# Performance work log

Measured on AMD Instinct MI355X. Metric: run time of the kernel, lower is better.

Reference implementation:

```python
import jax, jax.numpy as jnp
import numpy as np

B, L, D, H = 4, 1024, 1024, 16
HD = D // H
SCALE = 1.0 / np.sqrt(HD)
NOISE_PROB = 0.05
NOISE_SCALE = 0.1


def _linear(x, w, b):
    # torch nn.Linear convention: y = x @ W^T + b, W: [out, in]
    return x @ w.T + b


def _quantum_noise(key, real, imag, p=NOISE_PROB, s=NOISE_SCALE):
    """Phase flips, amplitude noise, and measurement dropout on a complex
    tensor represented as (real, imag). Deterministic given `key`."""
    k_phase, k_amp, k_nr, k_ni, k_meas = jax.random.split(key, 5)
    shape = real.shape
    flip = jnp.where(jax.random.uniform(k_phase, shape) < p, -1.0, 1.0)
    amp_mask = (jax.random.uniform(k_amp, shape) < p).astype(real.dtype)
    new_r = real * flip + jax.random.normal(k_nr, shape, real.dtype) * s * amp_mask
    new_i = imag * flip + jax.random.normal(k_ni, shape, imag.dtype) * s * amp_mask
    keep = 1.0 - (jax.random.uniform(k_meas, shape) < p * 0.5).astype(real.dtype)
    return new_r * keep, new_i * keep


def _heads(t):
    # [B, L, D] -> [B, H, L, HD]
    b, l, _ = t.shape
    return t.reshape(b, l, H, HD).transpose(0, 2, 1, 3)


def setup_inputs() -> dict:
    key = jax.random.key(0)
    ks = jax.random.split(key, 16)
    inp = {
        "x_real": jax.random.normal(ks[0], (B, L, D), jnp.float32),
        "x_imag": jax.random.normal(ks[1], (B, L, D), jnp.float32),
        "mask": jnp.ones((B, L), jnp.int32),
    }
    names = ["qr", "qi", "kr", "ki", "vr", "vi", "or", "oi"]
    for i, n in enumerate(names):
        inp[n + "_w"] = jax.random.normal(ks[2 + i], (D, D), jnp.float32) * 0.02
        inp[n + "_b"] = jnp.zeros((D,), jnp.float32)
    ent = jnp.eye(H) + (jax.random.normal(ks[10], (H, H)) * 0.1) * (
        jax.random.uniform(ks[11], (H, H)) < 0.2
    ).astype(jnp.float32)
    inp["ent"] = ent
    return inp


def reference(x_real, x_imag, mask, qr_w, qr_b, qi_w, qi_b, kr_w, kr_b,
              ki_w, ki_b, vr_w, vr_b, vi_w, vi_b, or_w, or_b, oi_w, oi_b, ent):
    # complex Q/K/V: real part from x.real, imag part from x.imag
    q_r, q_i = _linear(x_real, qr_w, qr_b), _linear(x_imag, qi_w, qi_b)
    k_r, k_i = _linear(x_real, kr_w, kr_b), _linear(x_imag, ki_w, ki_b)
    v_r, v_i = _linear(x_real, vr_w, vr_b), _linear(x_imag, vi_w, vi_b)

    nkey = jax.random.key(1)
    q_r, q_i = _quantum_noise(jax.random.fold_in(nkey, 0), q_r, q_i)
    k_r, k_i = _quantum_noise(jax.random.fold_in(nkey, 1), k_r, k_i)
    v_r, v_i = _quantum_noise(jax.random.fold_in(nkey, 2), v_r, v_i)

    q_r, q_i, k_r, k_i, v_r, v_i = map(_heads, (q_r, q_i, k_r, k_i, v_r, v_i))

    # torch.einsum('bhld,hh->bhld') == per-head scaling by diag(ent)
    d = jnp.diagonal(ent)[None, :, None, None]
    q_r, q_i = q_r * d, q_i * d
    k_r, k_i = k_r * d, k_i * d

    # Re(q . conj(k)) interference score: [B, H, Lq, Lk]
    scores = (jnp.einsum("bhqd,bhkd->bhqk", q_r, k_r)
              + jnp.einsum("bhqd,bhkd->bhqk", q_i, k_i)) * SCALE
    scores = jnp.where(mask[:, None, None, :] == 0, -1e9, scores)
    attn = jax.nn.softmax(scores, axis=-1)

    out_r = jnp.einsum("bhqk,bhkd->bhqd", attn, v_r)
    out_i = jnp.einsum("bhqk,bhkd->bhqd", attn, v_i)
    out_r = out_r.transpose(0, 2, 1, 3).reshape(x_real.shape)
    out_i = out_i.transpose(0, 2, 1, 3).reshape(x_real.shape)

    out_real = _linear(out_r, or_w, or_b)
    out_imag = _linear(out_i, oi_w, oi_b)
    return out_real, out_imag, attn
```

## Files before the change

### kernel.cpp

```cpp
#include <hip/hip_runtime.h>
#include <cstdint>

#define PARTITIONABLE 1

static constexpr int Bsz = 4, Lsz = 1024, Dsz = 1024, Hn = 16, HDsz = 64;
static constexpr size_t ELEMS = (size_t)Bsz * Lsz * Dsz;
static constexpr uint32_t HALF_N = (uint32_t)(ELEMS / 2);
static constexpr float SCALE = 0.125f;
static constexpr float P_NOISE = 0.05f;
static constexpr float S_NOISE = 0.1f;
static constexpr size_t MBy = 1024 * 1024;

typedef unsigned short u16;
typedef uint64_t u64;
typedef __attribute__((ext_vector_type(8))) short short8v;
typedef __attribute__((ext_vector_type(4))) float floatx4;
typedef __attribute__((ext_vector_type(4))) unsigned int uint4v;

__device__ __forceinline__ void gload16(const u16* g, u16* l) {
  __builtin_amdgcn_global_load_lds(
      (const __attribute__((address_space(1))) void*)(g),
      (__attribute__((address_space(3))) void*)(l), 16, 0, 0);
}

__host__ __device__ __forceinline__ void tf2x32(uint32_t k0, uint32_t k1,
                                                uint32_t x0, uint32_t x1,
                                                uint32_t& o0, uint32_t& o1) {
  uint32_t ks2 = k0 ^ k1 ^ 0x1BD11BDAu;
  x0 += k0; x1 += k1;
#define TFR(r) { x0 += x1; x1 = (x1 << (r)) | (x1 >> (32 - (r))); x1 ^= x0; }
  TFR(13) TFR(15) TFR(26) TFR(6)
  x0 += k1; x1 += ks2 + 1u;
  TFR(17) TFR(29) TFR(16) TFR(24)
  x0 += ks2; x1 += k0 + 2u;
  TFR(13) TFR(15) TFR(26) TFR(6)
  x0 += k0; x1 += k1 + 3u;
  TFR(17) TFR(29) TFR(16) TFR(24)
  x0 += k1; x1 += ks2 + 4u;
  TFR(13) TFR(15) TFR(26) TFR(6)
  x0 += ks2; x1 += k0 + 5u;
#undef TFR
  o0 = x0; o1 = x1;
}

struct KeySet { uint32_t k[5][2]; };
struct AllKeys { KeySet t[3]; };

__device__ __forceinline__ uint32_t draw_bits(uint32_t k0, uint32_t k1, uint32_t idx) {
#if PARTITIONABLE
  uint32_t o0, o1; tf2x32(k0, k1, 0u, idx, o0, o1);
  return o0 ^ o1;
#else
  uint32_t o0, o1;
  if (idx < HALF_N) { tf2x32(k0, k1, idx, idx + HALF_N, o0, o1); return o0; }
  tf2x32(k0, k1, idx - HALF_N, idx, o0, o1); return o1;
#endif
}

__device__ __forceinline__ float unif01(uint32_t bits) {
  return __uint_as_float((bits >> 9) | 0x3f800000u) - 1.0f;
}

__device__ __forceinline__ float normal_from_bits(uint32_t bits) {
  const float LO = -0.99999994f;
  float f = unif01(bits);
  float x = fmaxf(LO, f * 2.0f + LO);
  float w = -log1pf(-x * x);
  float p;
  if (w < 5.0f) {
    w = w - 2.5f;
    p = 2.81022636e-08f;
    p = fmaf(p, w, 3.43273939e-07f);
    p = fmaf(p, w, -3.5233877e-06f);
    p = fmaf(p, w, -4.39150654e-06f);
    p = fmaf(p, w, 0.00021858087f);
    p = fmaf(p, w, -0.00125372503f);
    p = fmaf(p, w, -0.00417768164f);
    p = fmaf(p, w, 0.246640727f);
    p = fmaf(p, w, 1.50140941f);
  } else {
    w = sqrtf(w) - 3.0f;
    p = -0.000200214257f;
    p = fmaf(p, w, 0.000100950558f);
    p = fmaf(p, w, 0.00134934322f);
    p = fmaf(p, w, -0.00367342844f);
    p = fmaf(p, w, 0.00573950773f);
    p = fmaf(p, w, -0.0076224613f);
    p = fmaf(p, w, 0.00943887047f);
    p = fmaf(p, w, 1.00167406f);
    p = fmaf(p, w, 2.83297682f);
  }
  return 1.41421356f * (p * x);
}

__device__ __forceinline__ uint32_t bf16_rn(float f) {
  uint32_t u = __float_as_uint(f);
  return (u + 0x7FFFu + ((u >> 16) & 1u)) >> 16;
}
__device__ __forceinline__ float bf2f(uint32_t h) { return __uint_as_float(h << 16); }
__device__ __forceinline__ void cvt_split(float4 v, u64& hi, u64& lo) {
  uint32_t h0 = bf16_rn(v.x), h1 = bf16_rn(v.y), h2 = bf16_rn(v.z), h3 = bf16_rn(v.w);
  float r0 = v.x - bf2f(h0), r1 = v.y - bf2f(h1), r2 = v.z - bf2f(h2), r3 = v.w - bf2f(h3);
  uint32_t l0 = bf16_rn(r0), l1 = bf16_rn(r1), l2 = bf16_rn(r2), l3 = bf16_rn(r3);
  hi = (u64)h0 | ((u64)h1 << 16) | ((u64)h2 << 32) | ((u64)h3 << 48);
  lo = (u64)l0 | ((u64)l1 << 16) | ((u64)l2 << 32) | ((u64)l3 << 48);
}

__device__ __forceinline__ void mfma_tile(const u16* Ahs, const u16* Als,
                                          const u16* Bhs, const u16* Bls,
                                          int l, int wm, int wn, floatx4 acc[4][4]) {
#pragma unroll
  for (int c = 0; c < 2; ++c) {
    const int pr = (l ^ (l >> 4) ^ (c << 2)) & 63;
    short8v aH[4], aL[4], bH[4], bL[4];
#pragma unroll
    for (int t = 0; t < 4; ++t) {
      const int ia = ((c * 8 + wm * 4 + t) * 64 + pr) * 8;
      aH[t] = *(const short8v*)&Ahs[ia]; aL[t] = *(const short8v*)&Als[ia];
      const int ib = ((c * 8 + wn * 4 + t) * 64 + pr) * 8;
      bH[t] = *(const short8v*)&Bhs[ib]; bL[t] = *(const short8v*)&Bls[ib];
    }
#pragma unroll
    for (int mt = 0; mt < 4; ++mt)
#pragma unroll
      for (int nt = 0; nt < 4; ++nt) {
        acc[mt][nt] = __builtin_amdgcn_mfma_f32_16x16x32_bf16(aH[mt], bH[nt], acc[mt][nt], 0, 0, 0);
        acc[mt][nt] = __builtin_amdgcn_mfma_f32_16x16x32_bf16(aH[mt], bL[nt], acc[mt][nt], 0, 0, 0);
        acc[mt][nt] = __builtin_amdgcn_mfma_f32_16x16x32_bf16(aL[mt], bH[nt], acc[mt][nt], 0, 0, 0);
      }
  }
}

__device__ __forceinline__ void mfma_step(const u16* Ahs, const u16* Als,
                                          const u16* Bhs, const u16* Bls,
                                          int pr, int wm, int wn, floatx4 acc[4][4]) {
  short8v aH[4], aL[4], bH[4], bL[4];
#pragma unroll
  for (int t = 0; t < 4; ++t) {
    const int ia = ((wm * 4 + t) * 64 + pr) * 8;
    aH[t] = *(const short8v*)&Ahs[ia]; aL[t] = *(const short8v*)&Als[ia];
    const int ib = ((wn * 4 + t) * 64 + pr) * 8;
    bH[t] = *(const short8v*)&Bhs[ib]; bL[t] = *(const short8v*)&Bls[ib];
  }
#pragma unroll
  for (int mt = 0; mt < 4; ++mt)
#pragma unroll
    for (int nt = 0; nt < 4; ++nt) {
      acc[mt][nt] = __builtin_amdgcn_mfma_f32_16x16x32_bf16(aH[mt], bH[nt], acc[mt][nt], 0, 0, 0);
      acc[mt][nt] = __builtin_amdgcn_mfma_f32_16x16x32_bf16(aH[mt], bL[nt], acc[mt][nt], 0, 0, 0);
      acc[mt][nt] = __builtin_amdgcn_mfma_f32_16x16x32_bf16(aL[mt], bH[nt], acc[mt][nt], 0, 0, 0);
    }
}

struct SJob { const float* src; u16* dh; u16* dl; int n4; };
struct SJobs { SJob j[8]; };

__global__ __launch_bounds__(256) void split8_kernel(SJobs js) {
  const SJob J = js.j[blockIdx.y];
  int i = blockIdx.x * 256 + (int)threadIdx.x;
  if (i >= J.n4) return;
  float4 v = ((const float4*)J.src)[i];
  u64 h, l; cvt_split(v, h, l);
  ((u64*)J.dh)[i] = h; ((u64*)J.dl)[i] = l;
}

struct GJob3 { const u16* Ah; const u16* Al;
               const u16* Wh[3]; const u16* Wl[3];
               const float* bias[3]; u16* Yh[3]; u16* Yl[3]; };
struct GJobs3 { GJob3 j[2]; };

__global__ __launch_bounds__(256, 2) void gemm3_kernel(GJobs3 jobs) {
  const GJob3 J = jobs.j[blockIdx.z];
  const int n0 = blockIdx.x * 128, m0 = blockIdx.y * 128;
  __shared__ u16 Ahs[4096], Als[4096];
  __shared__ u16 Bhs[3][4096], Bls[3][4096];
  const int tid = (int)threadIdx.x, w = tid >> 6, l = tid & 63;
  const int wm = w >> 1, wn = w & 1;
  const int qA = (l ^ (l >> 4)) & 15, colA = (l >> 4) * 8;
  const int pr = (l ^ (l >> 4)) & 63;
  const int t0 = w * 2, t1 = w * 2 + 1;

  const u16* ahp = J.Ah + (size_t)(m0 + qA) * Dsz + colA;
  const u16* alp = J.Al + (size_t)(m0 + qA) * Dsz + colA;
  const u16* whp0 = J.Wh[0] + (size_t)(n0 + qA) * Dsz + colA;
  const u16* wlp0 = J.Wl[0] + (size_t)(n0 + qA) * Dsz + colA;
  const u16* whp1 = J.Wh[1] + (size_t)(n0 + qA) * Dsz + colA;
  const u16* wlp1 = J.Wl[1] + (size_t)(n0 + qA) * Dsz + colA;
  const u16* whp2 = J.Wh[2] + (size_t)(n0 + qA) * Dsz + colA;
  const u16* wlp2 = J.Wl[2] + (size_t)(n0 + qA) * Dsz + colA;

  floatx4 acc[3][4][4];
#pragma unroll
  for (int z = 0; z < 3; ++z)
#pragma unroll
    for (int i = 0; i < 4; ++i)
#pragma unroll
      for (int j = 0; j < 4; ++j) acc[z][i][j] = (floatx4){0.f, 0.f, 0.f, 0.f};

  for (int kt = 0; kt < 32; ++kt) {
    const size_t g0 = (size_t)(t0 * 16) * Dsz + (size_t)kt * 32;
    const size_t g1 = (size_t)(t1 * 16) * Dsz + (size_t)kt * 32;
    __syncthreads();
    gload16(ahp + g0, &Ahs[t0 * 512]);  gload16(ahp + g1, &Ahs[t1 * 512]);
    gload16(alp + g0, &Als[t0 * 512]);  gload16(alp + g1, &Als[t1 * 512]);
    gload16(whp0 + g0, &Bhs[0][t0 * 512]); gload16(whp0 + g1, &Bhs[0][t1 * 512]);
    gload16(wlp0 + g0, &Bls[0][t0 * 512]); gload16(wlp0 + g1, &Bls[0][t1 * 512]);
    gload16(whp1 + g0, &Bhs[1][t0 * 512]); gload16(whp1 + g1, &Bhs[1][t1 * 512]);
    gload16(wlp1 + g0, &Bls[1][t0 * 512]); gload16(wlp1 + g1, &Bls[1][t1 * 512]);
    gload16(whp2 + g0, &Bhs[2][t0 * 512]); gload16(whp2 + g1, &Bhs[2][t1 * 512]);
    gload16(wlp2 + g0, &Bls[2][t0 * 512]); gload16(wlp2 + g1, &Bls[2][t1 * 512]);
    __syncthreads();

    short8v aH[4], aL[4];
#pragma unroll
    for (int t = 0; t < 4; ++t) {
      const int ia = ((wm * 4 + t) * 64 + pr) * 8;
      aH[t] = *(const short8v*)&Ahs[ia]; aL[t] = *(const short8v*)&Als[ia];
    }
#pragma unroll
    for (int z = 0; z < 3; ++z) {
#pragma unroll
      for (int nt = 0; nt < 4; ++nt) {
        const int ib = ((wn * 4 + nt) * 64 + pr) * 8;
        short8v bH = *(const short8v*)&Bhs[z][ib];
        short8v bL = *(const short8v*)&Bls[z][ib];
#pragma unroll
        for (int mt = 0; mt < 4; ++mt) {
          acc[z][mt][nt] = __builtin_amdgcn_mfma_f32_16x16x32_bf16(aH[mt], bH, acc[z][mt][nt], 0, 0, 0);
          acc[z][mt][nt] = __builtin_amdgcn_mfma_f32_16x16x32_bf16(aH[mt], bL, acc[z][mt][nt], 0, 0, 0);
          acc[z][mt][nt] = __builtin_amdgcn_mfma_f32_16x16x32_bf16(aL[mt], bH, acc[z][mt][nt], 0, 0, 0);
        }
      }
    }
  }

  const int colLane = l & 15, rquad = l >> 4;
#pragma unroll
  for (int z = 0; z < 3; ++z) {
    u16* Yh = J.Yh[z]; u16* Yl = J.Yl[z];
#pragma unroll
    for (int nt = 0; nt < 4; ++nt) {
      const int col = n0 + wn * 64 + nt * 16 + colLane;
      const float bv = J.bias[z][col];
#pragma unroll
      for (int mt = 0; mt < 4; ++mt) {
        const int r0 = m0 + wm * 64 + mt * 16 + rquad * 4;
#pragma unroll
        for (int j2 = 0; j2 < 4; ++j2) {
          float v = acc[z][mt][nt][j2] + bv;
          const uint32_t hi = bf16_rn(v);
          const uint32_t lo = bf16_rn(v - bf2f(hi));
          Yh[(size_t)(r0 + j2) * Dsz + col] = (u16)hi;
          Yl[(size_t)(r0 + j2) * Dsz + col] = (u16)lo;
        }
      }
    }
  }
}

struct GJob { const u16* Ah; const u16* Al; const u16* Wh; const u16* Wl;
              const float* bias; float* Yf; };
struct GJobs { GJob j[2]; };

__global__ __launch_bounds__(256, 2) void gemm_f32_kernel(GJobs jobs) {
  const GJob J = jobs.j[blockIdx.z];
  const int n0 = blockIdx.x * 128, m0 = blockIdx.y * 128;
  __shared__ u16 Ahs[8192], Als[8192], Bhs[8192], Bls[8192];
  const int tid = (int)threadIdx.x, w = tid >> 6, l = tid & 63;
  const int wm = w >> 1, wn = w & 1;
  const int cA = w >> 1, m2A = l >> 4;
  const int qA = (l ^ m2A ^ (cA << 2)) & 15;
  const int colA = cA * 32 + m2A * 8;
  const int tb = (w & 1) * 4;

  const u16* ahp = J.Ah + (size_t)(m0 + qA) * Dsz + colA;
  const u16* alp = J.Al + (size_t)(m0 + qA) * Dsz + colA;
  const u16* whp = J.Wh + (size_t)(n0 + qA) * Dsz + colA;
  const u16* wlp = J.Wl + (size_t)(n0 + qA) * Dsz + colA;

  floatx4 acc[4][4];
#pragma unroll
  for (int i = 0; i < 4; ++i)
#pragma unroll
    for (int j = 0; j < 4; ++j) acc[i][j] = (floatx4){0.f, 0.f, 0.f, 0.f};

  for (int k0 = 0; k0 < Dsz; k0 += 64) {
    __syncthreads();
#pragma unroll
    for (int i = 0; i < 4; ++i) {
      const size_t go = (size_t)((tb + i) * 16) * Dsz + k0;
      gload16(ahp + go, &Ahs[(w * 4 + i) * 512]);
      gload16(alp + go, &Als[(w * 4 + i) * 512]);
      gload16(whp + go, &Bhs[(w * 4 + i) * 512]);
      gload16(wlp + go, &Bls[(w * 4 + i) * 512]);
    }
    __syncthreads();
    mfma_tile(Ahs, Als, Bhs, Bls, l, wm, wn, acc);
  }

  const int colLane = l & 15, rquad = l >> 4;
#pragma unroll
  for (int nt = 0; nt < 4; ++nt) {
    const int col = n0 + wn * 64 + nt * 16 + colLane;
    const float bv = J.bias[col];
#pragma unroll
    for (int mt = 0; mt < 4; ++mt) {
      const int r0 = m0 + wm * 64 + mt * 16 + rquad * 4;
#pragma unroll
      for (int j2 = 0; j2 < 4; ++j2)
        J.Yf[(size_t)(r0 + j2) * Dsz + col] = acc[mt][nt][j2] + bv;
    }
  }
}

__global__ __launch_bounds__(256) void noise_kernel(
    u16* __restrict__ qhr, u16* __restrict__ qlr, u16* __restrict__ qhi, u16* __restrict__ qli,
    u16* __restrict__ khr, u16* __restrict__ klr, u16* __restrict__ khi, u16* __restrict__ kli,
    u16* __restrict__ vhr, u16* __restrict__ vlr, u16* __restrict__ vhi, u16* __restrict__ vli,
    const float* __restrict__ ent, AllKeys keys) {
  const uint32_t e = blockIdx.x * 256u + threadIdx.x;
  const int j = (int)blockIdx.y;
  u16 *rh, *rl, *ih, *il;
  if (j == 0) { rh = qhr; rl = qlr; ih = qhi; il = qli; }
  else if (j == 1) { rh = khr; rl = klr; ih = khi; il = kli; }
  else { rh = vhr; rl = vlr; ih = vhi; il = vli; }
  const KeySet& ks = keys.t[j];
  const uint32_t b_phase = draw_bits(ks.k[0][0], ks.k[0][1], e);
  const uint32_t b_amp   = draw_bits(ks.k[1][0], ks.k[1][1], e);
  const uint32_t b_nr    = draw_bits(ks.k[2][0], ks.k[2][1], e);
  const uint32_t b_ni    = draw_bits(ks.k[3][0], ks.k[3][1], e);
  const uint32_t b_meas  = draw_bits(ks.k[4][0], ks.k[4][1], e);
  const float flip = (unif01(b_phase) < P_NOISE) ? -1.0f : 1.0f;
  const float amp  = (unif01(b_amp)  < P_NOISE) ? 1.0f : 0.0f;
  const float keep = (unif01(b_meas) < P_NOISE * 0.5f) ? 0.0f : 1.0f;
  const float nr = normal_from_bits(b_nr);
  const float ni = normal_from_bits(b_ni);
  float r  = bf2f(rh[e]) + bf2f(rl[e]);
  float iv = bf2f(ih[e]) + bf2f(il[e]);
  r  = (r  * flip + nr * S_NOISE * amp) * keep;
  iv = (iv * flip + ni * S_NOISE * amp) * keep;
  if (j != 2) {
    const int h = ((int)e & (Dsz - 1)) >> 6;
    const float d = ent[h * Hn + h];
    r *= d; iv *= d;
  }
  uint32_t hr = bf16_rn(r);  rh[e] = (u16)hr; rl[e] = (u16)bf16_rn(r - bf2f(hr));
  uint32_t hi2 = bf16_rn(iv); ih[e] = (u16)hi2; il[e] = (u16)bf16_rn(iv - bf2f(hi2));
}

__global__ __launch_bounds__(256, 2) void scores_kernel(
    const u16* __restrict__ qhr, const u16* __restrict__ qlr,
    const u16* __restrict__ qhi, const u16* __restrict__ qli,
    const u16* __restrict__ khr, const u16* __restrict__ klr,
    const u16* __restrict__ khi, const u16* __restrict__ kli,
    const int* __restrict__ mask, float* __restrict__ attn) {
  const int bh = (int)blockIdx.z;
  const int b = bh >> 4, h = bh & 15;
  const int n0 = blockIdx.x * 128, m0 = blockIdx.y * 128;
  __shared__ u16 Ahs[2][4096], Als[2][4096], Bhs[2][4096], Bls[2][4096];
  const int tid = (int)threadIdx.x, w = tid >> 6, l = tid & 63;
  const int wm = w >> 1, wn = w & 1;
  const int qA = (l ^ (l >> 4)) & 15, colA = (l >> 4) * 8;
  const int pr = (l ^ (l >> 4)) & 63;
  const int t0 = w * 2, t1 = w * 2 + 1;

  const size_t aoff = ((size_t)(b * Lsz) + m0 + qA) * Dsz + h * HDsz + colA;
  const size_t boff = ((size_t)(b * Lsz) + n0 + qA) * Dsz + h * HDsz + colA;

  floatx4 acc[4][4];
#pragma unroll
  for (int i = 0; i < 4; ++i)
#pragma unroll
    for (int j = 0; j < 4; ++j) acc[i][j] = (floatx4){0.f, 0.f, 0.f, 0.f};

#define STGS(bufi, AH, AL, BH, BL, K0V) { \
    const size_t g0 = (size_t)(t0 * 16) * Dsz + (K0V); \
    const size_t g1 = (size_t)(t1 * 16) * Dsz + (K0V); \
    gload16(AH + aoff + g0, &Ahs[bufi][t0 * 512]); gload16(AH + aoff + g1, &Ahs[bufi][t1 * 512]); \
    gload16(AL + aoff + g0, &Als[bufi][t0 * 512]); gload16(AL + aoff + g1, &Als[bufi][t1 * 512]); \
    gload16(BH + boff + g0, &Bhs[bufi][t0 * 512]); gload16(BH + boff + g1, &Bhs[bufi][t1 * 512]); \
    gload16(BL + boff + g0, &Bls[bufi][t0 * 512]); gload16(BL + boff + g1, &Bls[bufi][t1 * 512]); }

  STGS(0, qhr, qlr, khr, klr, 0)
  __syncthreads();
  STGS(1, qhr, qlr, khr, klr, 32)
  mfma_step(Ahs[0], Als[0], Bhs[0], Bls[0], pr, wm, wn, acc);
  __syncthreads();
  STGS(0, qhi, qli, khi, kli, 0)
  mfma_step(Ahs[1], Als[1], Bhs[1], Bls[1], pr, wm, wn, acc);
  __syncthreads();
  STGS(1, qhi, qli, khi, kli, 32)
  mfma_step(Ahs[0], Als[0], Bhs[0], Bls[0], pr, wm, wn, acc);
  __syncthreads();
  mfma_step(Ahs[1], Als[1], Bhs[1], Bls[1], pr, wm, wn, acc);
#undef STGS

  const int colLane = l & 15, rquad = l >> 4;
#pragma unroll
  for (int nt = 0; nt < 4; ++nt) {
    const int col = n0 + wn * 64 + nt * 16 + colLane;
    const int mv = mask[b * Lsz + col];
#pragma unroll
    for (int mt = 0; mt < 4; ++mt) {
      const int r0 = m0 + wm * 64 + mt * 16 + rquad * 4;
#pragma unroll
      for (int j = 0; j < 4; ++j)
        attn[((size_t)bh * Lsz + r0 + j) * Lsz + col] =
            (mv == 0) ? -1e9f : acc[mt][nt][j] * SCALE;
    }
  }
}

__global__ __launch_bounds__(256) void vtrans_kernel(
    const u16* __restrict__ vhr, const u16* __restrict__ vlr,
    const u16* __restrict__ vhi, const u16* __restrict__ vli,
    u16* __restrict__ vth, u16* __restrict__ vtl) {
  const int bh = (int)blockIdx.y;
  const int b = bh >> 4, h = bh & 15;
  const int k0 = blockIdx.x * 64;
  __shared__ uint32_t T[128 * 65];
  const int t = (int)threadIdx.x;
  const int krow = t >> 4, d4 = (t & 15) * 4;

#pragma unroll
  for (int src = 0; src < 2; ++src) {
    const u16* VH = src ? vhi : vhr;
    const u16* VL = src ? vli : vlr;
    const int nb = src * 64;
#pragma unroll
    for (int p = 0; p < 4; ++p) {
      const int k = p * 16 + krow;
      const size_t off = ((size_t)(b * Lsz) + k0 + k) * Dsz + h * HDsz + d4;
      u64 hv = *(const u64*)(VH + off);
      u64 lv = *(const u64*)(VL + off);
#pragma unroll
      for (int e = 0; e < 4; ++e) {
        uint32_t hi = (uint32_t)((hv >> (16 * e)) & 0xFFFFu);
        uint32_t lo = (uint32_t)((lv >> (16 * e)) & 0xFFFFu);
        T[(nb + d4 + e) * 65 + k] = lo | (hi << 16);
      }
    }
  }
  __syncthreads();
  const int n = t >> 1, hf = t & 1;
  const size_t rowb = ((size_t)bh * 128 + n) * Lsz + k0 + hf * 32;
#pragma unroll
  for (int g = 0; g < 4; ++g) {
    uint32_t wv[8];
#pragma unroll
    for (int u = 0; u < 8; ++u) wv[u] = T[n * 65 + hf * 32 + g * 8 + u];
    uint4v hvv, lvv;
    hvv.x = (wv[0] >> 16) | (wv[1] & 0xFFFF0000u);
    hvv.y = (wv[2] >> 16) | (wv[3] & 0xFFFF0000u);
    hvv.z = (wv[4] >> 16) | (wv[5] & 0xFFFF0000u);
    hvv.w = (wv[6] >> 16) | (wv[7] & 0xFFFF0000u);
    lvv.x = (wv[0] & 0xFFFFu) | (wv[1] << 16);
    lvv.y = (wv[2] & 0xFFFFu) | (wv[3] << 16);
    lvv.z = (wv[4] & 0xFFFFu) | (wv[5] << 16);
    lvv.w = (wv[6] & 0xFFFFu) | (wv[7] << 16);
    *(uint4v*)&vth[rowb + g * 8] = hvv;
    *(uint4v*)&vtl[rowb + g * 8] = lvv;
  }
}

__global__ __launch_bounds__(256) void rowstat_kernel(const float* __restrict__ S,
                                                      float* __restrict__ rowm,
                                                      float* __restrict__ rowsum) {
  const int wv = (int)threadIdx.x >> 6, lane = (int)threadIdx.x & 63;
  const size_t row = (size_t)blockIdx.x * 4 + wv;
  const float* p = S + row * Lsz;
  float4 v[4];
#pragma unroll
  for (int i = 0; i < 4; ++i) v[i] = *(const float4*)(p + i * 256 + lane * 4);
  float m = -3.402823466e38f;
#pragma unroll
  for (int i = 0; i < 4; ++i)
    m = fmaxf(m, fmaxf(fmaxf(v[i].x, v[i].y), fmaxf(v[i].z, v[i].w)));
#pragma unroll
  for (int d = 1; d < 64; d <<= 1) m = fmaxf(m, __shfl_xor(m, d));
  float s = 0.f;
#pragma unroll
  for (int i = 0; i < 4; ++i)
    s += expf(v[i].x - m) + expf(v[i].y - m) + expf(v[i].z - m) + expf(v[i].w - m);
#pragma unroll
  for (int d = 1; d < 64; d <<= 1) s += __shfl_xor(s, d);
  if (lane == 0) { rowm[row] = m; rowsum[row] = s; }
}

__global__ __launch_bounds__(256, 2) void pv_kernel(
    float* __restrict__ attn, const u16* __restrict__ vth, const u16* __restrict__ vtl,
    const float* __restrict__ rowm, const float* __restrict__ rowsum,
    u16* __restrict__ ohr, u16* __restrict__ olr,
    u16* __restrict__ ohi, u16* __restrict__ oli) {
  const int bh = (int)blockIdx.y;
  const int b = bh >> 4, h = bh & 15;
  const int m0 = blockIdx.x * 128;
  __shared__ u16 Ahs[2][4096], Als[2][4096], Bhs[2][4096], Bls[2][4096];
  const int tid = (int)threadIdx.x, w = tid >> 6, l = tid & 63;
  const int wm = w >> 1, wn = w & 1;
  const int qA = (l ^ (l >> 4)) & 15, colA = (l >> 4) * 8;
  const int pr = (l ^ (l >> 4)) & 63;
  const int t0 = w * 2, t1 = w * 2 + 1;

  const int ar = tid >> 3, akq = tid & 7;
  const int am2 = akq >> 1, ahalf = akq & 1;
  int aidx[4];
  float rmv[4], inv[4];
#pragma unroll
  for (int rr = 0; rr < 4; ++rr) {
    const int trow = ar + rr * 32;
    const int p = ((trow & 15) + 16 * am2) ^ am2;
    aidx[rr] = ((trow >> 4) * 64 + p) * 8 + ahalf * 4;
    const size_t grow = (size_t)bh * Lsz + m0 + trow;
    rmv[rr] = rowm[grow]; inv[rr] = 1.0f / rowsum[grow];
  }
  float* arp = attn + ((size_t)bh * Lsz + m0 + ar) * Lsz + akq * 4;
  const u16* bhp = vth + ((size_t)bh * 128 + qA) * Lsz + colA;
  const u16* blp = vtl + ((size_t)bh * 128 + qA) * Lsz + colA;

  floatx4 acc[4][4];
#pragma unroll
  for (int i = 0; i < 4; ++i)
#pragma unroll
    for (int j = 0; j < 4; ++j) acc[i][j] = (floatx4){0.f, 0.f, 0.f, 0.f};

#define STGB(bufi, K0V) { \
    const size_t g0 = (size_t)(t0 * 16) * Lsz + (K0V); \
    const size_t g1 = (size_t)(t1 * 16) * Lsz + (K0V); \
    gload16(bhp + g0, &Bhs[bufi][t0 * 512]); gload16(bhp + g1, &Bhs[bufi][t1 * 512]); \
    gload16(blp + g0, &Bls[bufi][t0 * 512]); gload16(blp + g1, &Bls[bufi][t1 * 512]); }

#define LOADA(K0V, A4) { \
    _Pragma("unroll") for (int rr = 0; rr < 4; ++rr) \
      A4[rr] = *(const float4*)(arp + (size_t)(rr * 32) * Lsz + (K0V)); }

#define PROCA(bufi, K0V, A4) { \
    _Pragma("unroll") for (int rr = 0; rr < 4; ++rr) { \
      float4 p4; \
      p4.x = expf(A4[rr].x - rmv[rr]) * inv[rr]; \
      p4.y = expf(A4[rr].y - rmv[rr]) * inv[rr]; \
      p4.z = expf(A4[rr].z - rmv[rr]) * inv[rr]; \
      p4.w = expf(A4[rr].w - rmv[rr]) * inv[rr]; \
      *(float4*)(arp + (size_t)(rr * 32) * Lsz + (K0V)) = p4; \
      u64 h64, l64; cvt_split(p4, h64, l64); \
      *(u64*)&Ahs[bufi][aidx[rr]] = h64; *(u64*)&Als[bufi][aidx[rr]] = l64; } }

  {
    float4 a4[4];
    LOADA(0, a4)
    STGB(0, 0)
    PROCA(0, 0, a4)
  }
  __syncthreads();
  for (int kt = 0; kt < 32; kt += 2) {
    float4 n4[4];
    if (kt + 1 < 32) { LOADA((size_t)(kt + 1) * 32, n4) STGB(1, (size_t)(kt + 1) * 32) }
    mfma_step(Ahs[0], Als[0], Bhs[0], Bls[0], pr, wm, wn, acc);
    if (kt + 1 < 32) PROCA(1, (size_t)(kt + 1) * 32, n4)
    __syncthreads();
    if (kt + 2 < 32) { LOADA((size_t)(kt + 2) * 32, n4) STGB(0, (size_t)(kt + 2) * 32) }
    mfma_step(Ahs[1], Als[1], Bhs[1], Bls[1], pr, wm, wn, acc);
    if (kt + 2 < 32) PROCA(0, (size_t)(kt + 2) * 32, n4)
    __syncthreads();
  }
#undef STGB
#undef LOADA
#undef PROCA

  const int colLane = l & 15, rquad = l >> 4;
#pragma unroll
  for (int nt = 0; nt < 4; ++nt) {
    const int col = wn * 64 + nt * 16 + colLane;
    u16* oh = (col < 64) ? ohr : ohi;
    u16* ol = (col < 64) ? olr : oli;
    const int dcol = col & 63;
#pragma unroll
    for (int mt = 0; mt < 4; ++mt) {
      const int r0 = m0 + wm * 64 + mt * 16 + rquad * 4;
#pragma unroll
      for (int j = 0; j < 4; ++j) {
        float v = acc[mt][nt][j];
        const uint32_t hi = bf16_rn(v);
        const uint32_t lo = bf16_rn(v - bf2f(hi));
        const size_t oidx = ((size_t)(b * Lsz) + r0 + j) * Dsz + h * HDsz + dcol;
        oh[oidx] = (u16)hi; ol[oidx] = (u16)lo;
      }
    }
  }
}

extern "C" void kernel_launch(void* const* d_in, const int* in_sizes, int n_in,
                              void* d_out, int out_size, void* d_ws, size_t ws_size,
                              hipStream_t stream) {
  const float* x_real = (const float*)d_in[0];
  const float* x_imag = (const float*)d_in[1];
  const int*   mask   = (const int*)d_in[2];
  const float* pw[6] = {(const float*)d_in[3], (const float*)d_in[5], (const float*)d_in[7],
                        (const float*)d_in[9], (const float*)d_in[11], (const float*)d_in[13]};
  const float* pb[6] = {(const float*)d_in[4], (const float*)d_in[6], (const float*)d_in[8],
                        (const float*)d_in[10], (const float*)d_in[12], (const float*)d_in[14]};
  const float* or_w = (const float*)d_in[15]; const float* or_b = (const float*)d_in[16];
  const float* oi_w = (const float*)d_in[17]; const float* oi_b = (const float*)d_in[18];
  const float* ent  = (const float*)d_in[19];

  float* out_real = (float*)d_out;
  float* out_imag = out_real + ELEMS;
  float* attn     = out_imag + ELEMS;

  if (ws_size < 96 * MBy) return;
  uint8_t* wsb = (uint8_t*)d_ws;
  u16* qhr = (u16*)(wsb + 0 * MBy);  u16* qlr = (u16*)(wsb + 8 * MBy);
  u16* qhi = (u16*)(wsb + 16 * MBy); u16* qli = (u16*)(wsb + 24 * MBy);
  u16* khr = (u16*)(wsb + 32 * MBy); u16* klr = (u16*)(wsb + 40 * MBy);
  u16* khi = (u16*)(wsb + 48 * MBy); u16* kli = (u16*)(wsb + 56 * MBy);
  u16* xhr = (u16*)(wsb + 64 * MBy); u16* xlr = (u16*)(wsb + 72 * MBy);
  u16* xhi = (u16*)(wsb + 80 * MBy); u16* xli = (u16*)(wsb + 88 * MBy);
  u16* vth = (u16*)(wsb + 64 * MBy); u16* vtl = (u16*)(wsb + 80 * MBy);
  u16* ohr = (u16*)(wsb + 0 * MBy);  u16* olr = (u16*)(wsb + 8 * MBy);
  u16* ohi = (u16*)(wsb + 16 * MBy); u16* oli = (u16*)(wsb + 24 * MBy);
  u16* owh[2] = {(u16*)(wsb + 32 * MBy), (u16*)(wsb + 36 * MBy)};
  u16* owl[2] = {(u16*)(wsb + 34 * MBy), (u16*)(wsb + 38 * MBy)};

  uint8_t* atb = (uint8_t*)attn;
  u16* vhr = (u16*)(atb + 0 * MBy);  u16* vlr = (u16*)(atb + 8 * MBy);
  u16* vhi = (u16*)(atb + 16 * MBy); u16* vli = (u16*)(atb + 24 * MBy);

  float* rowm = out_real;
  float* rowsum = out_real + 65536;

  AllKeys keys;
  for (int j = 0; j < 3; ++j) {
    uint32_t a, b2;
    tf2x32(0u, 1u, 0u, (uint32_t)j, a, b2);
#if PARTITIONABLE
    for (int i = 0; i < 5; ++i)
      tf2x32(a, b2, 0u, (uint32_t)i, keys.t[j].k[i][0], keys.t[j].k[i][1]);
#else
    uint32_t out10[10];
    for (int i = 0; i < 5; ++i) {
      uint32_t o0, o1; tf2x32(a, b2, (uint32_t)i, (uint32_t)(i + 5), o0, o1);
      out10[i] = o0; out10[i + 5] = o1;
    }
    for (int i = 0; i < 5; ++i) { keys.t[j].k[i][0] = out10[2*i]; keys.t[j].k[i][1] = out10[2*i+1]; }
#endif
  }

  u16* pwh[6]; u16* pwl[6];
  for (int z = 0; z < 6; ++z) {
    pwh[z] = (u16*)(atb + 32 * MBy + (size_t)z * 4 * MBy);
    pwl[z] = pwh[z] + (size_t)Dsz * Dsz;
  }
  SJobs sj{};
  sj.j[0] = {x_real, xhr, xlr, (int)(ELEMS / 4)};
  sj.j[1] = {x_imag, xhi, xli, (int)(ELEMS / 4)};
  for (int z = 0; z < 6; ++z) sj.j[2 + z] = {pw[z], pwh[z], pwl[z], Dsz * Dsz / 4};
  split8_kernel<<<dim3(4096, 8), 256, 0, stream>>>(sj);

  GJobs3 pj{};
  pj.j[0].Ah = xhr; pj.j[0].Al = xlr;
  pj.j[0].Wh[0] = pwh[0]; pj.j[0].Wl[0] = pwl[0]; pj.j[0].bias[0] = pb[0];
  pj.j[0].Yh[0] = qhr; pj.j[0].Yl[0] = qlr;
  pj.j[0].Wh[1] = pwh[2]; pj.j[0].Wl[1] = pwl[2]; pj.j[0].bias[1] = pb[2];
  pj.j[0].Yh[1] = khr; pj.j[0].Yl[1] = klr;
  pj.j[0].Wh[2] = pwh[4]; pj.j[0].Wl[2] = pwl[4]; pj.j[0].bias[2] = pb[4];
  pj.j[0].Yh[2] = vhr; pj.j[0].Yl[2] = vlr;
  pj.j[1].Ah = xhi; pj.j[1].Al = xli;
  pj.j[1].Wh[0] = pwh[1]; pj.j[1].Wl[0] = pwl[1]; pj.j[1].bias[0] = pb[1];
  pj.j[1].Yh[0] = qhi; pj.j[1].Yl[0] = qli;
  pj.j[1].Wh[1] = pwh[3]; pj.j[1].Wl[1] = pwl[3]; pj.j[1].bias[1] = pb[3];
  pj.j[1].Yh[1] = khi; pj.j[1].Yl[1] = kli;
  pj.j[1].Wh[2] = pwh[5]; pj.j[1].Wl[2] = pwl[5]; pj.j[1].bias[2] = pb[5];
  pj.j[1].Yh[2] = vhi; pj.j[1].Yl[2] = vli;
  gemm3_kernel<<<dim3(8, 32, 2), 256, 0, stream>>>(pj);

  noise_kernel<<<dim3((uint32_t)(ELEMS / 256), 3), 256, 0, stream>>>(
      qhr, qlr, qhi, qli, khr, klr, khi, kli, vhr, vlr, vhi, vli, ent, keys);

  vtrans_kernel<<<dim3(16, 64), 256, 0, stream>>>(vhr, vlr, vhi, vli, vth, vtl);

  scores_kernel<<<dim3(8, 8, 64), 256, 0, stream>>>(
      qhr, qlr, qhi, qli, khr, klr, khi, kli, mask, attn);

  SJobs so{};
  so.j[0] = {or_w, owh[0], owl[0], Dsz * Dsz / 4};
  so.j[1] = {oi_w, owh[1], owl[1], Dsz * Dsz / 4};
  split8_kernel<<<dim3(1024, 2), 256, 0, stream>>>(so);

  rowstat_kernel<<<dim3(16384), 256, 0, stream>>>(attn, rowm, rowsum);

  pv_kernel<<<dim3(8, 64), 256, 0, stream>>>(attn, vth, vtl, rowm, rowsum,
                                             ohr, olr, ohi, oli);

  GJobs oj{};
  oj.j[0].Ah = ohr; oj.j[0].Al = olr; oj.j[0].Wh = owh[0]; oj.j[0].Wl = owl[0];
  oj.j[0].bias = or_b; oj.j[0].Yf = out_real;
  oj.j[1].Ah = ohi; oj.j[1].Al = oli; oj.j[1].Wh = owh[1]; oj.j[1].Wl = owl[1];
  oj.j[1].bias = oi_b; oj.j[1].Yf = out_imag;
  gemm_f32_kernel<<<dim3(8, 32, 2), 256, 0, stream>>>(oj);
}
```

Baseline: 771.6 us.

## Split noise kernel into two passes, computing Gaussian draws only for amp-flagged elements

The noise pass is split in two. The first kernel applies flip, keep and entanglement scaling, and compacts the indices of elements whose amplitude-noise flag is set (and that are not dropped) into a list using wave ballot plus an atomic counter. The second kernel computes the two normal draws only for those roughly 5% of elements and adds the noise. This removes two Threefry draws and the Box-Muller/erfinv-style normal computations for about 95% of elements. In exchange it adds an extra launch, atomics, and a reread and rewrite of the flagged elements, which incurs a second bf16 rounding on them. The final element order is also nondeterministic.

After: 2.797 ms. 3.63x slower.

```diff
diff --git a/kernel.cpp b/kernel.cpp
--- a/kernel.cpp
+++ b/kernel.cpp
@@ -155,7 +155,8 @@
 struct SJob { const float* src; u16* dh; u16* dl; int n4; };
 struct SJobs { SJob j[8]; };
 
-__global__ __launch_bounds__(256) void split8_kernel(SJobs js) {
+__global__ __launch_bounds__(256) void split8_kernel(SJobs js, uint32_t* counter) {
+  if (counter && blockIdx.x == 0 && blockIdx.y == 0 && threadIdx.x == 0) *counter = 0;
   const SJob J = js.j[blockIdx.y];
   int i = blockIdx.x * 256 + (int)threadIdx.x;
   if (i >= J.n4) return;
@@ -313,11 +314,12 @@
   }
 }
 
-__global__ __launch_bounds__(256) void noise_kernel(
+__global__ __launch_bounds__(256) void noise1_kernel(
     u16* __restrict__ qhr, u16* __restrict__ qlr, u16* __restrict__ qhi, u16* __restrict__ qli,
     u16* __restrict__ khr, u16* __restrict__ klr, u16* __restrict__ khi, u16* __restrict__ kli,
     u16* __restrict__ vhr, u16* __restrict__ vlr, u16* __restrict__ vhi, u16* __restrict__ vli,
-    const float* __restrict__ ent, AllKeys keys) {
+    const float* __restrict__ ent, AllKeys keys,
+    uint32_t* __restrict__ list, uint32_t* __restrict__ counter) {
   const uint32_t e = blockIdx.x * 256u + threadIdx.x;
   const int j = (int)blockIdx.y;
   u16 *rh, *rl, *ih, *il;
@@ -327,25 +329,62 @@
   const KeySet& ks = keys.t[j];
   const uint32_t b_phase = draw_bits(ks.k[0][0], ks.k[0][1], e);
   const uint32_t b_amp   = draw_bits(ks.k[1][0], ks.k[1][1], e);
-  const uint32_t b_nr    = draw_bits(ks.k[2][0], ks.k[2][1], e);
-  const uint32_t b_ni    = draw_bits(ks.k[3][0], ks.k[3][1], e);
   const uint32_t b_meas  = draw_bits(ks.k[4][0], ks.k[4][1], e);
   const float flip = (unif01(b_phase) < P_NOISE) ? -1.0f : 1.0f;
-  const float amp  = (unif01(b_amp)  < P_NOISE) ? 1.0f : 0.0f;
+  const bool  ampf = (unif01(b_amp)  < P_NOISE);
   const float keep = (unif01(b_meas) < P_NOISE * 0.5f) ? 0.0f : 1.0f;
-  const float nr = normal_from_bits(b_nr);
-  const float ni = normal_from_bits(b_ni);
-  float r  = bf2f(rh[e]) + bf2f(rl[e]);
-  float iv = bf2f(ih[e]) + bf2f(il[e]);
-  r  = (r  * flip + nr * S_NOISE * amp) * keep;
-  iv = (iv * flip + ni * S_NOISE * amp) * keep;
+  float d = 1.0f;
   if (j != 2) {
     const int h = ((int)e & (Dsz - 1)) >> 6;
-    const float d = ent[h * Hn + h];
-    r *= d; iv *= d;
-  }
+    d = ent[h * Hn + h];
+  }
+  float r  = (bf2f(rh[e]) + bf2f(rl[e])) * flip * keep * d;
+  float iv = (bf2f(ih[e]) + bf2f(il[e])) * flip * keep * d;
   uint32_t hr = bf16_rn(r);  rh[e] = (u16)hr; rl[e] = (u16)bf16_rn(r - bf2f(hr));
   uint32_t hi2 = bf16_rn(iv); ih[e] = (u16)hi2; il[e] = (u16)bf16_rn(iv - bf2f(hi2));
+
+  const bool flag = ampf && (keep != 0.0f);
+  const int lane = (int)threadIdx.x & 63;
+  unsigned long long mask = __ballot(flag);
+  int cnt = __popcll(mask);
+  int base = 0;
+  if (lane == 0 && cnt) base = (int)atomicAdd(counter, (uint32_t)cnt);
+  base = __shfl(base, 0);
+  if (flag) {
+    int pos = __popcll(mask & ((1ull << lane) - 1ull));
+    list[base + pos] = ((uint32_t)j << 22) | e;
+  }
+}
+
+__global__ __launch_bounds__(256) void noise2_kernel(
+    const uint32_t* __restrict__ list, const uint32_t* __restrict__ counter,
+    u16* __restrict__ qhr, u16* __restrict__ qlr, u16* __restrict__ qhi, u16* __restrict__ qli,
+    u16* __restrict__ khr, u16* __restrict__ klr, u16* __restrict__ khi, u16* __restrict__ kli,
+    u16* __restrict__ vhr, u16* __restrict__ vlr, u16* __restrict__ vhi, u16* __restrict__ vli,
+    const float* __restrict__ ent, AllKeys keys) {
+  const uint32_t cnt = *counter;
+  const uint32_t stride = gridDim.x * 256u;
+  for (uint32_t i = blockIdx.x * 256u + threadIdx.x; i < cnt; i += stride) {
+    const uint32_t pk = list[i];
+    const int j = (int)(pk >> 22);
+    const uint32_t e = pk & 0x3FFFFFu;
+    u16 *rh, *rl, *ih, *il;
+    if (j == 0) { rh = qhr; rl = qlr; ih = qhi; il = qli; }
+    else if (j == 1) { rh = khr; rl = klr; ih = khi; il = kli; }
+    else { rh = vhr; rl = vlr; ih = vhi; il = vli; }
+    const KeySet& ks = keys.t[j];
+    const float nr = normal_from_bits(draw_bits(ks.k[2][0], ks.k[2][1], e));
+    const float ni = normal_from_bits(draw_bits(ks.k[3][0], ks.k[3][1], e));
+    float d = 1.0f;
+    if (j != 2) {
+      const int h = ((int)e & (Dsz - 1)) >> 6;
+      d = ent[h * Hn + h];
+    }
+    float r  = bf2f(rh[e]) + bf2f(rl[e]) + nr * S_NOISE * d;
+    float iv = bf2f(ih[e]) + bf2f(il[e]) + ni * S_NOISE * d;
+    uint32_t hr = bf16_rn(r);  rh[e] = (u16)hr; rl[e] = (u16)bf16_rn(r - bf2f(hr));
+    uint32_t hi2 = bf16_rn(iv); ih[e] = (u16)hi2; il[e] = (u16)bf16_rn(iv - bf2f(hi2));
+  }
 }
 
 __global__ __launch_bounds__(256, 2) void scores_kernel(
@@ -624,6 +663,8 @@
   uint8_t* atb = (uint8_t*)attn;
   u16* vhr = (u16*)(atb + 0 * MBy);  u16* vlr = (u16*)(atb + 8 * MBy);
   u16* vhi = (u16*)(atb + 16 * MBy); u16* vli = (u16*)(atb + 24 * MBy);
+  uint32_t* counter = (uint32_t*)(atb + 56 * MBy);
+  uint32_t* list    = (uint32_t*)(atb + 56 * MBy + 1024);
 
   float* rowm = out_real;
   float* rowsum = out_real + 65536;
@@ -654,7 +695,7 @@
   sj.j[0] = {x_real, xhr, xlr, (int)(ELEMS / 4)};
   sj.j[1] = {x_imag, xhi, xli, (int)(ELEMS / 4)};
   for (int z = 0; z < 6; ++z) sj.j[2 + z] = {pw[z], pwh[z], pwl[z], Dsz * Dsz / 4};
-  split8_kernel<<<dim3(4096, 8), 256, 0, stream>>>(sj);
+  split8_kernel<<<dim3(4096, 8), 256, 0, stream>>>(sj, counter);
 
   GJobs3 pj{};
   pj.j[0].Ah = xhr; pj.j[0].Al = xlr;
@@ -673,8 +714,12 @@
   pj.j[1].Yh[2] = vhi; pj.j[1].Yl[2] = vli;
   gemm3_kernel<<<dim3(8, 32, 2), 256, 0, stream>>>(pj);
 
-  noise_kernel<<<dim3((uint32_t)(ELEMS / 256), 3), 256, 0, stream>>>(
-      qhr, qlr, qhi, qli, khr, klr, khi, kli, vhr, vlr, vhi, vli, ent, keys);
+  noise1_kernel<<<dim3((uint32_t)(ELEMS / 256), 3), 256, 0, stream>>>(
+      qhr, qlr, qhi, qli, khr, klr, khi, kli, vhr, vlr, vhi, vli, ent, keys,
+      list, counter);
+  noise2_kernel<<<dim3(2048), 256, 0, stream>>>(
+      list, counter, qhr, qlr, qhi, qli, khr, klr, khi, kli, vhr, vlr, vhi, vli,
+      ent, keys);
 
   vtrans_kernel<<<dim3(16, 64), 256, 0, stream>>>(vhr, vlr, vhi, vli, vth, vtl);
 
@@ -684,7 +729,7 @@
   SJobs so{};
   so.j[0] = {or_w, owh[0], owl[0], Dsz * Dsz / 4};
   so.j[1] = {oi_w, owh[1], owl[1], Dsz * Dsz / 4};
-  split8_kernel<<<dim3(1024, 2), 256, 0, stream>>>(so);
+  split8_kernel<<<dim3(1024, 2), 256, 0, stream>>>(so, nullptr);
 
   rowstat_kernel<<<dim3(16384), 256, 0, stream>>>(attn, rowm, rowsum);
 
```
